# Performance work log

Measured on AMD Instinct MI355X. Metric: run time of the kernel, lower is better.

## Reference

```python
import jax, jax.numpy as jnp
import numpy as np

N_GRAPHS, NODES_PER, DEG, D = 128, 1024, 32, 256
N = N_GRAPHS * NODES_PER          # 131072 nodes
E = N * DEG                       # 4194304 edges
RATIO = 0.8
K = int(np.ceil(RATIO * NODES_PER))  # 820 nodes kept per graph


def setup_inputs() -> dict:
    key = jax.random.key(0)
    k1, k2, k3, k4 = jax.random.split(key, 4)
    x = jax.random.normal(k1, (N, D), dtype=jnp.float32)
    # intra-graph random edges: endpoints within [0, NODES_PER) + graph offset
    src = jax.random.randint(k2, (E,), 0, NODES_PER)
    dst = jax.random.randint(k3, (E,), 0, NODES_PER)
    goff = (jnp.arange(E) // (NODES_PER * DEG)) * NODES_PER
    edge_index = jnp.stack([src + goff, dst + goff]).astype(jnp.int32)
    batch = jnp.repeat(jnp.arange(N_GRAPHS, dtype=jnp.int32), NODES_PER)
    W = jax.random.normal(k4, (D, 1), dtype=jnp.float32) / np.sqrt(D)
    b = jnp.zeros((1,), dtype=jnp.float32)
    return {"x": x, "edge_index": edge_index, "batch": batch, "W": W, "b": b}


def _gcn_score(x, edge_index, W, b):
    # GCNConv(in_channels, 1) with added self-loops and symmetric normalization
    n = x.shape[0]
    row, col = edge_index[0], edge_index[1]  # source, target
    # degree at target, init 1.0 accounts for self-loop
    deg = jnp.ones((n,), x.dtype).at[col].add(jnp.ones_like(col, dtype=x.dtype))
    dinv = jax.lax.rsqrt(deg)
    h = x @ W                                 # [n, 1]
    norm = dinv[row] * dinv[col]              # [E]
    agg = jnp.zeros_like(h).at[col].add(norm[:, None] * h[row])
    agg = agg + (dinv * dinv)[:, None] * h    # self-loop contribution deg^-1 * h_i
    return (agg + b).squeeze(-1)              # [n]


def reference(x, edge_index, batch, W, b):
    score = _gcn_score(x, edge_index, W, b)                     # [N]
    # per-graph top-k (graphs are contiguous, equal size)
    score_g = score.reshape(N_GRAPHS, NODES_PER)
    _, idx = jax.lax.top_k(score_g, K)                          # [G, K]
    perm = (idx + jnp.arange(N_GRAPHS)[:, None] * NODES_PER).reshape(-1)  # [G*K]
    x_new = x[perm] * jnp.tanh(score[perm])[:, None]            # [G*K, D]
    batch_new = batch[perm]
    # filter_adj: remap kept nodes to new ids, mask edges with dropped endpoints
    new_id = jnp.full((x.shape[0],), -1, dtype=perm.dtype).at[perm].set(
        jnp.arange(perm.shape[0], dtype=perm.dtype))
    r2 = new_id[edge_index[0]]
    c2 = new_id[edge_index[1]]
    edge_mask = (r2 >= 0) & (c2 >= 0)                           # [E] valid edges
    edge_index_new = jnp.where(edge_mask, jnp.stack([r2, c2]), -1)  # [2, E], -1 = dropped
    return x_new, edge_index_new, edge_mask, batch_new, perm
```

## Files before the change

kernel.cpp:

```cpp
#include <hip/hip_runtime.h>
#include <math.h>

constexpr int NG    = 128;
constexpr int NP    = 1024;
constexpr int D     = 256;
constexpr int NTOT  = NG * NP;
constexpr int EPG   = NP * 32;
constexpr int ET    = NTOT * 32;
constexpr int KK    = 820;
constexpr int NKEEP = NG * KK;

constexpr long long OUT_X     = 0;
constexpr long long OUT_EI0   = (long long)NKEEP * D;
constexpr long long OUT_EI1   = OUT_EI0 + ET;
constexpr long long OUT_MASK  = OUT_EI0 + 2LL * ET;
constexpr long long OUT_BATCH = OUT_MASK + ET;
constexpr long long OUT_PERM  = OUT_BATCH + NKEEP;

__global__ void node_init_kernel(const float* __restrict__ x,
                                 const float* __restrict__ W,
                                 float* __restrict__ h,
                                 int* __restrict__ new_id) {
    int row  = blockIdx.x * 4 + (threadIdx.x >> 6);
    int lane = threadIdx.x & 63;
    float4 a = ((const float4*)(x + (size_t)row * D))[lane];
    float4 w = ((const float4*)W)[lane];
    float s = a.x * w.x + a.y * w.y + a.z * w.z + a.w * w.w;
#pragma unroll
    for (int off = 32; off > 0; off >>= 1) s += __shfl_down(s, off, 64);
    if (lane == 0) {
        h[row]      = s;
        new_id[row] = -1;
    }
}

__global__ __launch_bounds__(1024) void graph_kernel(
        const int* __restrict__ rows, const int* __restrict__ cols,
        const float* __restrict__ h, const float* __restrict__ b,
        int* __restrict__ perm_i, int* __restrict__ new_id,
        float* __restrict__ factor,
        float* __restrict__ out_perm, float* __restrict__ out_batch) {
    __shared__ float hl[NP];
    __shared__ float uu[NP];
    __shared__ float acc[NP];
    __shared__ int   degc[NP];
    __shared__ unsigned long long sk[NP];

    const int g = blockIdx.x;
    const int t = threadIdx.x;
    const int nbase = g * NP;

    hl[t]   = h[nbase + t];
    degc[t] = 1;
    __syncthreads();

    const int4* c4 = (const int4*)(cols + (size_t)g * EPG);
    const int4* r4 = (const int4*)(rows + (size_t)g * EPG);

#pragma unroll
    for (int i = t; i < EPG / 4; i += 1024) {
        int4 c = c4[i];
        atomicAdd(&degc[c.x & (NP - 1)], 1);
        atomicAdd(&degc[c.y & (NP - 1)], 1);
        atomicAdd(&degc[c.z & (NP - 1)], 1);
        atomicAdd(&degc[c.w & (NP - 1)], 1);
    }
    __syncthreads();

    float di = rsqrtf((float)degc[t]);
    uu[t]  = di * hl[t];
    acc[t] = 0.0f;
    __syncthreads();

#pragma unroll
    for (int i = t; i < EPG / 4; i += 1024) {
        int4 c = c4[i];
        int4 r = r4[i];
        atomicAdd(&acc[c.x & (NP - 1)], uu[r.x & (NP - 1)]);
        atomicAdd(&acc[c.y & (NP - 1)], uu[r.y & (NP - 1)]);
        atomicAdd(&acc[c.z & (NP - 1)], uu[r.z & (NP - 1)]);
        atomicAdd(&acc[c.w & (NP - 1)], uu[r.w & (NP - 1)]);
    }
    __syncthreads();

    float score = di * acc[t] + di * di * hl[t] + b[0];
    hl[t] = score;

    unsigned int fu = __float_as_uint(score);
    unsigned int s  = (fu & 0x80000000u) ? ~fu : (fu | 0x80000000u);
    unsigned long long key = ((unsigned long long)(~s) << 32) | (unsigned int)t;

    for (int k = 2; k <= NP; k <<= 1) {
        for (int j = k >> 1; j > 0; j >>= 1) {
            unsigned long long other;
            if (j < 64) {
                other = __shfl_xor(key, j, 64);
            } else {
                sk[t] = key;
                __syncthreads();
                other = sk[t ^ j];
                __syncthreads();
            }
            bool take_min = (((t & k) == 0) == ((t & j) == 0));
            bool omin = other < key;
            key = (take_min == omin) ? other : key;
        }
    }

    if (t < KK) {
        int idx  = (int)(key & 0xFFFFFFFFull);
        int node = nbase + idx;
        int j    = g * KK + t;
        perm_i[j]    = node;
        new_id[node] = j;
        out_perm[j]  = (float)node;
        out_batch[j] = (float)g;
        factor[j]    = tanhf(hl[idx]);
    }
}

__global__ void gather_kernel(const float* __restrict__ x,
                              const int* __restrict__ perm_i,
                              const float* __restrict__ factor,
                              float* __restrict__ out_x) {
    int j    = blockIdx.x * 4 + (threadIdx.x >> 6);
    int lane = threadIdx.x & 63;
    int node = perm_i[j];
    float t  = factor[j];
    float4 v = ((const float4*)(x + (size_t)node * D))[lane];
    float4 o = make_float4(v.x * t, v.y * t, v.z * t, v.w * t);
    ((float4*)(out_x + (size_t)j * D))[lane] = o;
}

__global__ void edge_kernel(const int* __restrict__ row, const int* __restrict__ col,
                            const int* __restrict__ new_id,
                            float* __restrict__ out_r, float* __restrict__ out_c,
                            float* __restrict__ out_m) {
    int t = blockIdx.x * blockDim.x + threadIdx.x;
    int4 r = ((const int4*)row)[t];
    int4 c = ((const int4*)col)[t];
    float4 fr, fc, fm;
    {
        int nr = new_id[r.x], nc = new_id[c.x];
        bool m = (nr >= 0) && (nc >= 0);
        fr.x = m ? (float)nr : -1.0f; fc.x = m ? (float)nc : -1.0f; fm.x = m ? 1.0f : 0.0f;
    }
    {
        int nr = new_id[r.y], nc = new_id[c.y];
        bool m = (nr >= 0) && (nc >= 0);
        fr.y = m ? (float)nr : -1.0f; fc.y = m ? (float)nc : -1.0f; fm.y = m ? 1.0f : 0.0f;
    }
    {
        int nr = new_id[r.z], nc = new_id[c.z];
        bool m = (nr >= 0) && (nc >= 0);
        fr.z = m ? (float)nr : -1.0f; fc.z = m ? (float)nc : -1.0f; fm.z = m ? 1.0f : 0.0f;
    }
    {
        int nr = new_id[r.w], nc = new_id[c.w];
        bool m = (nr >= 0) && (nc >= 0);
        fr.w = m ? (float)nr : -1.0f; fc.w = m ? (float)nc : -1.0f; fm.w = m ? 1.0f : 0.0f;
    }
    ((float4*)out_r)[t] = fr;
    ((float4*)out_c)[t] = fc;
    ((float4*)out_m)[t] = fm;
}

extern "C" void kernel_launch(void* const* d_in, const int* in_sizes, int n_in,
                              void* d_out, int out_size, void* d_ws, size_t ws_size,
                              hipStream_t stream) {
    const float* x  = (const float*)d_in[0];
    const int*   ei = (const int*)d_in[1];
    const float* W  = (const float*)d_in[3];
    const float* b  = (const float*)d_in[4];
    float* out = (float*)d_out;

    float* wsf    = (float*)d_ws;
    float* h      = wsf;
    int*   new_id = (int*)wsf + NTOT;
    int*   perm_i = (int*)wsf + 2 * NTOT;
    float* factor = wsf + 2 * NTOT + NKEEP;

    const int* rows = ei;
    const int* cols = ei + ET;

    hipLaunchKernelGGL(node_init_kernel, dim3(NTOT / 4), dim3(256), 0, stream,
                       x, W, h, new_id);
    hipLaunchKernelGGL(graph_kernel, dim3(NG), dim3(1024), 0, stream,
                       rows, cols, h, b, perm_i, new_id, factor,
                       out + OUT_PERM, out + OUT_BATCH);
    hipLaunchKernelGGL(gather_kernel, dim3(NKEEP / 4), dim3(256), 0, stream,
                       x, perm_i, factor, out + OUT_X);
    hipLaunchKernelGGL(edge_kernel, dim3(ET / 4 / 256), dim3(256), 0, stream,
                       rows, cols, new_id, out + OUT_EI0, out + OUT_EI1, out + OUT_MASK);
}
```

Baseline: 355.9 us.

## Split per-graph scoring across four blocks per graph and stage edge remap via LDS

The single 128-block graph kernel is split into a degree-count kernel and a normalized-aggregation kernel. Each runs 512 blocks, with each block covering a quarter of a graph's edges and writing per-block partial results to workspace. A separate sort kernel sums the four partials and runs the bitonic top-k. The edge remap kernel now loads each graph's new_id table into shared memory, so lookups no longer go to global memory, but it launches only 512 blocks instead of thousands. The aim is more GPU parallelism for the edge scans, at the cost of extra launches, partial-buffer traffic and lower occupancy in the edge pass.

```diff
diff --git a/kernel.cpp b/kernel.cpp
--- a/kernel.cpp
+++ b/kernel.cpp
@@ -9,6 +9,9 @@
 constexpr int ET    = NTOT * 32;
 constexpr int KK    = 820;
 constexpr int NKEEP = NG * KK;
+constexpr int BPG   = 4;
+constexpr int EPB   = EPG / BPG;
+constexpr int NBE   = NG * BPG;
 
 constexpr long long OUT_X     = 0;
 constexpr long long OUT_EI0   = (long long)NKEEP * D;
@@ -34,57 +37,80 @@
     }
 }
 
-__global__ __launch_bounds__(1024) void graph_kernel(
-        const int* __restrict__ rows, const int* __restrict__ cols,
+__global__ __launch_bounds__(256) void deg_part_kernel(const int* __restrict__ cols,
+                                                       int* __restrict__ deg_part) {
+    __shared__ int cnt[NP];
+    const int b = blockIdx.x;
+    const int g = b >> 2;
+    for (int i = threadIdx.x; i < NP; i += 256) cnt[i] = 0;
+    __syncthreads();
+    const int4* c4 = (const int4*)(cols + (size_t)g * EPG + (size_t)(b & 3) * EPB);
+#pragma unroll
+    for (int i = threadIdx.x; i < EPB / 4; i += 256) {
+        int4 c = c4[i];
+        atomicAdd(&cnt[c.x & (NP - 1)], 1);
+        atomicAdd(&cnt[c.y & (NP - 1)], 1);
+        atomicAdd(&cnt[c.z & (NP - 1)], 1);
+        atomicAdd(&cnt[c.w & (NP - 1)], 1);
+    }
+    __syncthreads();
+    int* dst = deg_part + (size_t)b * NP;
+    for (int i = threadIdx.x; i < NP; i += 256) dst[i] = cnt[i];
+}
+
+__global__ __launch_bounds__(256) void acc_part_kernel(const int* __restrict__ rows,
+                                                       const int* __restrict__ cols,
+                                                       const float* __restrict__ h,
+                                                       const int* __restrict__ deg_part,
+                                                       float* __restrict__ acc_part) {
+    __shared__ float ul[NP];
+    __shared__ float acc[NP];
+    const int b = blockIdx.x;
+    const int g = b >> 2;
+    const int* dp = deg_part + (size_t)g * BPG * NP;
+    for (int i = threadIdx.x; i < NP; i += 256) {
+        int d = 1 + dp[i] + dp[NP + i] + dp[2 * NP + i] + dp[3 * NP + i];
+        ul[i]  = rsqrtf((float)d) * h[g * NP + i];
+        acc[i] = 0.0f;
+    }
+    __syncthreads();
+    size_t eoff = (size_t)g * EPG + (size_t)(b & 3) * EPB;
+    const int4* c4 = (const int4*)(cols + eoff);
+    const int4* r4 = (const int4*)(rows + eoff);
+#pragma unroll
+    for (int i = threadIdx.x; i < EPB / 4; i += 256) {
+        int4 c = c4[i];
+        int4 r = r4[i];
+        atomicAdd(&acc[c.x & (NP - 1)], ul[r.x & (NP - 1)]);
+        atomicAdd(&acc[c.y & (NP - 1)], ul[r.y & (NP - 1)]);
+        atomicAdd(&acc[c.z & (NP - 1)], ul[r.z & (NP - 1)]);
+        atomicAdd(&acc[c.w & (NP - 1)], ul[r.w & (NP - 1)]);
+    }
+    __syncthreads();
+    float* dst = acc_part + (size_t)b * NP;
+    for (int i = threadIdx.x; i < NP; i += 256) dst[i] = acc[i];
+}
+
+__global__ __launch_bounds__(1024) void sort_kernel(
         const float* __restrict__ h, const float* __restrict__ b,
+        const int* __restrict__ deg_part, const float* __restrict__ acc_part,
         int* __restrict__ perm_i, int* __restrict__ new_id,
         float* __restrict__ factor,
         float* __restrict__ out_perm, float* __restrict__ out_batch) {
-    __shared__ float hl[NP];
-    __shared__ float uu[NP];
-    __shared__ float acc[NP];
-    __shared__ int   degc[NP];
     __shared__ unsigned long long sk[NP];
+    __shared__ float scl[NP];
 
     const int g = blockIdx.x;
     const int t = threadIdx.x;
-    const int nbase = g * NP;
-
-    hl[t]   = h[nbase + t];
-    degc[t] = 1;
-    __syncthreads();
-
-    const int4* c4 = (const int4*)(cols + (size_t)g * EPG);
-    const int4* r4 = (const int4*)(rows + (size_t)g * EPG);
-
-#pragma unroll
-    for (int i = t; i < EPG / 4; i += 1024) {
-        int4 c = c4[i];
-        atomicAdd(&degc[c.x & (NP - 1)], 1);
-        atomicAdd(&degc[c.y & (NP - 1)], 1);
-        atomicAdd(&degc[c.z & (NP - 1)], 1);
-        atomicAdd(&degc[c.w & (NP - 1)], 1);
-    }
-    __syncthreads();
-
-    float di = rsqrtf((float)degc[t]);
-    uu[t]  = di * hl[t];
-    acc[t] = 0.0f;
-    __syncthreads();
-
-#pragma unroll
-    for (int i = t; i < EPG / 4; i += 1024) {
-        int4 c = c4[i];
-        int4 r = r4[i];
-        atomicAdd(&acc[c.x & (NP - 1)], uu[r.x & (NP - 1)]);
-        atomicAdd(&acc[c.y & (NP - 1)], uu[r.y & (NP - 1)]);
-        atomicAdd(&acc[c.z & (NP - 1)], uu[r.z & (NP - 1)]);
-        atomicAdd(&acc[c.w & (NP - 1)], uu[r.w & (NP - 1)]);
-    }
-    __syncthreads();
-
-    float score = di * acc[t] + di * di * hl[t] + b[0];
-    hl[t] = score;
+    const int*   dp = deg_part + (size_t)g * BPG * NP;
+    const float* ap = acc_part + (size_t)g * BPG * NP;
+
+    int   d  = 1 + dp[t] + dp[NP + t] + dp[2 * NP + t] + dp[3 * NP + t];
+    float av = ap[t] + ap[NP + t] + ap[2 * NP + t] + ap[3 * NP + t];
+    float hv = h[g * NP + t];
+    float di = rsqrtf((float)d);
+    float score = di * av + di * di * hv + b[0];
+    scl[t] = score;
 
     unsigned int fu = __float_as_uint(score);
     unsigned int s  = (fu & 0x80000000u) ? ~fu : (fu | 0x80000000u);
@@ -109,13 +135,13 @@
 
     if (t < KK) {
         int idx  = (int)(key & 0xFFFFFFFFull);
-        int node = nbase + idx;
+        int node = g * NP + idx;
         int j    = g * KK + t;
         perm_i[j]    = node;
         new_id[node] = j;
         out_perm[j]  = (float)node;
         out_batch[j] = (float)g;
-        factor[j]    = tanhf(hl[idx]);
+        factor[j]    = tanhf(scl[idx]);
     }
 }
 
@@ -132,37 +158,52 @@
     ((float4*)(out_x + (size_t)j * D))[lane] = o;
 }
 
-__global__ void edge_kernel(const int* __restrict__ row, const int* __restrict__ col,
-                            const int* __restrict__ new_id,
-                            float* __restrict__ out_r, float* __restrict__ out_c,
-                            float* __restrict__ out_m) {
-    int t = blockIdx.x * blockDim.x + threadIdx.x;
-    int4 r = ((const int4*)row)[t];
-    int4 c = ((const int4*)col)[t];
-    float4 fr, fc, fm;
-    {
-        int nr = new_id[r.x], nc = new_id[c.x];
-        bool m = (nr >= 0) && (nc >= 0);
-        fr.x = m ? (float)nr : -1.0f; fc.x = m ? (float)nc : -1.0f; fm.x = m ? 1.0f : 0.0f;
-    }
-    {
-        int nr = new_id[r.y], nc = new_id[c.y];
-        bool m = (nr >= 0) && (nc >= 0);
-        fr.y = m ? (float)nr : -1.0f; fc.y = m ? (float)nc : -1.0f; fm.y = m ? 1.0f : 0.0f;
-    }
-    {
-        int nr = new_id[r.z], nc = new_id[c.z];
-        bool m = (nr >= 0) && (nc >= 0);
-        fr.z = m ? (float)nr : -1.0f; fc.z = m ? (float)nc : -1.0f; fm.z = m ? 1.0f : 0.0f;
-    }
-    {
-        int nr = new_id[r.w], nc = new_id[c.w];
-        bool m = (nr >= 0) && (nc >= 0);
-        fr.w = m ? (float)nr : -1.0f; fc.w = m ? (float)nc : -1.0f; fm.w = m ? 1.0f : 0.0f;
-    }
-    ((float4*)out_r)[t] = fr;
-    ((float4*)out_c)[t] = fc;
-    ((float4*)out_m)[t] = fm;
+__global__ __launch_bounds__(256) void edge_kernel(const int* __restrict__ rows,
+                                                   const int* __restrict__ cols,
+                                                   const int* __restrict__ new_id,
+                                                   float* __restrict__ out_r,
+                                                   float* __restrict__ out_c,
+                                                   float* __restrict__ out_m) {
+    __shared__ int nid[NP];
+    const int b = blockIdx.x;
+    const int g = b >> 2;
+    for (int i = threadIdx.x; i < NP; i += 256) nid[i] = new_id[g * NP + i];
+    __syncthreads();
+    size_t eoff = (size_t)g * EPG + (size_t)(b & 3) * EPB;
+    const int4* r4 = (const int4*)(rows + eoff);
+    const int4* c4 = (const int4*)(cols + eoff);
+    float4* orr = (float4*)(out_r + eoff);
+    float4* occ = (float4*)(out_c + eoff);
+    float4* omm = (float4*)(out_m + eoff);
+#pragma unroll
+    for (int i = threadIdx.x; i < EPB / 4; i += 256) {
+        int4 r = r4[i];
+        int4 c = c4[i];
+        float4 fr, fc, fm;
+        {
+            int nr = nid[r.x & (NP - 1)], nc = nid[c.x & (NP - 1)];
+            bool m = (nr >= 0) && (nc >= 0);
+            fr.x = m ? (float)nr : -1.0f; fc.x = m ? (float)nc : -1.0f; fm.x = m ? 1.0f : 0.0f;
+        }
+        {
+            int nr = nid[r.y & (NP - 1)], nc = nid[c.y & (NP - 1)];
+            bool m = (nr >= 0) && (nc >= 0);
+            fr.y = m ? (float)nr : -1.0f; fc.y = m ? (float)nc : -1.0f; fm.y = m ? 1.0f : 0.0f;
+        }
+        {
+            int nr = nid[r.z & (NP - 1)], nc = nid[c.z & (NP - 1)];
+            bool m = (nr >= 0) && (nc >= 0);
+            fr.z = m ? (float)nr : -1.0f; fc.z = m ? (float)nc : -1.0f; fm.z = m ? 1.0f : 0.0f;
+        }
+        {
+            int nr = nid[r.w & (NP - 1)], nc = nid[c.w & (NP - 1)];
+            bool m = (nr >= 0) && (nc >= 0);
+            fr.w = m ? (float)nr : -1.0f; fc.w = m ? (float)nc : -1.0f; fm.w = m ? 1.0f : 0.0f;
+        }
+        orr[i] = fr;
+        occ[i] = fc;
+        omm[i] = fm;
+    }
 }
 
 extern "C" void kernel_launch(void* const* d_in, const int* in_sizes, int n_in,
@@ -174,22 +215,28 @@
     const float* b  = (const float*)d_in[4];
     float* out = (float*)d_out;
 
-    float* wsf    = (float*)d_ws;
-    float* h      = wsf;
-    int*   new_id = (int*)wsf + NTOT;
-    int*   perm_i = (int*)wsf + 2 * NTOT;
-    float* factor = wsf + 2 * NTOT + NKEEP;
+    float* wsf      = (float*)d_ws;
+    float* h        = wsf;
+    int*   new_id   = (int*)wsf + NTOT;
+    int*   perm_i   = (int*)wsf + 2 * NTOT;
+    float* factor   = wsf + 2 * NTOT + NKEEP;
+    int*   deg_part = (int*)wsf + 2 * NTOT + 2 * NKEEP;
+    float* acc_part = wsf + 2 * NTOT + 2 * NKEEP + NBE * NP;
 
     const int* rows = ei;
     const int* cols = ei + ET;
 
     hipLaunchKernelGGL(node_init_kernel, dim3(NTOT / 4), dim3(256), 0, stream,
                        x, W, h, new_id);
-    hipLaunchKernelGGL(graph_kernel, dim3(NG), dim3(1024), 0, stream,
-                       rows, cols, h, b, perm_i, new_id, factor,
+    hipLaunchKernelGGL(deg_part_kernel, dim3(NBE), dim3(256), 0, stream,
+                       cols, deg_part);
+    hipLaunchKernelGGL(acc_part_kernel, dim3(NBE), dim3(256), 0, stream,
+                       rows, cols, h, deg_part, acc_part);
+    hipLaunchKernelGGL(sort_kernel, dim3(NG), dim3(1024), 0, stream,
+                       h, b, deg_part, acc_part, perm_i, new_id, factor,
                        out + OUT_PERM, out + OUT_BATCH);
     hipLaunchKernelGGL(gather_kernel, dim3(NKEEP / 4), dim3(256), 0, stream,
                        x, perm_i, factor, out + OUT_X);
-    hipLaunchKernelGGL(edge_kernel, dim3(ET / 4 / 256), dim3(256), 0, stream,
+    hipLaunchKernelGGL(edge_kernel, dim3(NBE), dim3(256), 0, stream,
                        rows, cols, new_id, out + OUT_EI0, out + OUT_EI1, out + OUT_MASK);
 }
```

Result: faster. 336.1 us (-5.6%).
